# Kernel optimization log

Measured on AMD Instinct MI355X. Metric: run time of the kernel, lower is better.

The kernel has to match this reference:

```python
import jax, jax.numpy as jnp
import numpy as np

N, E = 50000, 800000
FN, FE, D, H = 64, 16, 128, 4


def setup_inputs() -> dict:
    key = jax.random.key(0)
    ks = jax.random.split(key, 16)
    inp = {
        "nodes": jax.random.normal(ks[0], (N, FN), jnp.float32),
        "edges": jax.random.normal(ks[1], (E, FE), jnp.float32),
        "senders": jax.random.randint(ks[2], (E,), 0, N, jnp.int32),
        "receivers": jax.random.randint(ks[3], (E,), 0, N, jnp.int32),
        "avg_multi_head": 0,
        # params (orthogonal init approximated by scaled normal; math identical)
        "W_node": jax.random.normal(ks[4], (FN, D), jnp.float32) / np.sqrt(FN),
        "b_node": jnp.zeros((D,), jnp.float32),
        "W_edge": jax.random.normal(ks[5], (FE, D), jnp.float32) / np.sqrt(FE),
        "b_edge": jnp.zeros((D,), jnp.float32),
        "Wk_s": jax.random.normal(ks[6], (H, D, D), jnp.float32) / np.sqrt(D),
        "bk_s": jnp.zeros((H, D), jnp.float32),
        "Wk_r": jax.random.normal(ks[7], (H, D, D), jnp.float32) / np.sqrt(D),
        "bk_r": jnp.zeros((H, D), jnp.float32),
        "W_out": jax.random.normal(ks[8], (H * D, D), jnp.float32) / np.sqrt(H * D),
        "b_out": jnp.zeros((D,), jnp.float32),
    }
    return inp


def _segment_softmax(logits, seg_ids, num_segments):
    seg_max = jax.ops.segment_max(logits, seg_ids, num_segments=num_segments)
    seg_max = jnp.where(jnp.isfinite(seg_max), seg_max, 0.0)  # empty segments
    e = jnp.exp(logits - seg_max[seg_ids])
    seg_sum = jax.ops.segment_sum(e, seg_ids, num_segments=num_segments)
    return e / seg_sum[seg_ids]


def reference(nodes, edges, senders, receivers, avg_multi_head,
              W_node, b_node, W_edge, b_edge, Wk_s, bk_s, Wk_r, bk_r,
              W_out, b_out):
    n_node = nodes.shape[0]
    x = nodes @ W_node + b_node            # [N, D] projected nodes
    ef = edges @ W_edge + b_edge           # [E, D] projected edge features
    sa = x[senders]                        # [E, D] sent attributes
    ra = x[receivers]                      # [E, D] received attributes
    scale = 1.0 / jnp.sqrt(jnp.asarray(D, x.dtype))
    heads = []
    for h in range(H):  # small fixed head count, structurally distinct params
        k_s = sa @ Wk_s[h] + bk_s[h]                 # [E, D]
        k_r = ra @ Wk_r[h] + bk_r[h] + ef            # [E, D]
        logits = jnp.sum(k_s * k_r, axis=1) * scale  # [E]
        w = _segment_softmax(logits, receivers, n_node)
        msg = w[:, None] * (sa + ef)                 # [E, D]
        heads.append(jax.ops.segment_sum(msg, receivers, num_segments=n_node))
    if avg_multi_head:
        agg = jnp.mean(jnp.stack(heads), axis=0)
    else:
        agg = jnp.concatenate(heads, axis=1) @ W_out + b_out
    return jax.nn.relu(x + agg)            # new node features [N, D]
```

## Files before the change

### kernel.cpp

```cpp
#include <hip/hip_runtime.h>

typedef unsigned short u16;
typedef unsigned int u32;
typedef short bh8 __attribute__((ext_vector_type(8)));
typedef float f4 __attribute__((ext_vector_type(4)));
typedef float pf2 __attribute__((ext_vector_type(2)));

__device__ __forceinline__ float bf2f(u16 h) { return __uint_as_float(((u32)h) << 16); }
__device__ __forceinline__ float bflo(u32 u) { return __uint_as_float(u << 16); }
__device__ __forceinline__ float bfhi(u32 u) { return __uint_as_float(u & 0xffff0000u); }
__device__ __forceinline__ u16 f2bf(float f) {
    u32 x = __float_as_uint(f);
    return (u16)((x + 0x7fffu + ((x >> 16) & 1u)) >> 16);
}
__device__ __forceinline__ pf2 pkfma(pf2 a, pf2 b, pf2 c) {
    pf2 d;
    asm("v_pk_fma_f32 %0, %1, %2, %3" : "=v"(d) : "v"(a), "v"(b), "v"(c));
    return d;
}
__device__ __forceinline__ pf2 u2f2(u32 u) {
    pf2 r;
    r.x = bflo(u);
    r.y = bfhi(u);
    return r;
}
__device__ __forceinline__ float dpp_red16(float x) {
    int y;
    y = __builtin_amdgcn_update_dpp(0, __float_as_int(x), 0xB1, 0xF, 0xF, true);
    x += __int_as_float(y);
    y = __builtin_amdgcn_update_dpp(0, __float_as_int(x), 0x4E, 0xF, 0xF, true);
    x += __int_as_float(y);
    y = __builtin_amdgcn_update_dpp(0, __float_as_int(x), 0x141, 0xF, 0xF, true);
    x += __int_as_float(y);
    y = __builtin_amdgcn_update_dpp(0, __float_as_int(x), 0x140, 0xF, 0xF, true);
    x += __int_as_float(y);
    return x;
}

#define KSCL 0.12751744336457488f

__global__ void k0a_kernel(const float* __restrict__ Wn, const float* __restrict__ Wks,
                           const float* __restrict__ Wkr, float* __restrict__ A,
                           float* __restrict__ B) {
    int idx = blockIdx.x * 256 + threadIdx.x;
    if (idx >= 65536) return;
    int which = idx >> 15;
    int rem = idx & 32767;
    int h = rem >> 13;
    int r = rem & 8191;
    int a = r >> 7, dp = r & 127;
    const float* W = which ? Wks : Wkr;
    float acc = 0.f;
    for (int d = 0; d < 128; ++d)
        acc += Wn[a * 128 + d] * W[(h * 128 + d) * 128 + dp];
    (which ? B : A)[(h * 64 + a) * 128 + dp] = acc;
}

__global__ void k0a2_kernel(const float* __restrict__ bn, const float* __restrict__ Wks,
                            const float* __restrict__ Wkr, const float* __restrict__ bks,
                            const float* __restrict__ bkr, float* __restrict__ ybs,
                            float* __restrict__ ybr) {
    int idx = blockIdx.x * 256 + threadIdx.x;
    if (idx >= 1024) return;
    int which = idx >> 9;
    int rem = idx & 511;
    int h = rem >> 7, dp = rem & 127;
    const float* W = which ? Wks : Wkr;
    const float* b = which ? bks : bkr;
    float acc = b[h * 128 + dp];
    for (int d = 0; d < 128; ++d) acc += bn[d] * W[(h * 128 + d) * 128 + dp];
    (which ? ybs : ybr)[h * 128 + dp] = acc;
}

__global__ void k0b_kernel(const float* __restrict__ Wn, const float* __restrict__ bn,
                           const float* __restrict__ A, const float* __restrict__ B,
                           const float* __restrict__ ybr, const float* __restrict__ ybs,
                           const float* __restrict__ Wks, const float* __restrict__ Wedge,
                           const float* __restrict__ bks, const float* __restrict__ bedge,
                           float* __restrict__ Wfold, float* __restrict__ biasrow) {
    int idx = blockIdx.x * 256 + threadIdx.x;
    if (idx >= 65 * 708) return;
    int a = idx / 708, c = idx % 708;
    float val;
    if (c < 128) {
        val = (a < 64) ? Wn[a * 128 + c] : bn[c];
    } else if (c < 640) {
        int h = (c - 128) >> 7, i = (c - 128) & 127;
        const float* rv = (a < 64) ? &A[(h * 64 + a) * 128] : &ybr[h * 128];
        float s = 0.f;
        for (int d = 0; d < 128; ++d) s += rv[d] * Wks[(h * 128 + i) * 128 + d];
        val = s;
    } else if (c < 704) {
        int k = (c - 640) >> 2, h = (c - 640) & 3;
        const float* rv = (a < 64) ? &B[(h * 64 + a) * 128] : &ybs[h * 128];
        float s = 0.f;
        for (int d = 0; d < 128; ++d) s += rv[d] * Wedge[k * 128 + d];
        val = s;
    } else {
        int h = c - 704;
        const float* rv = (a < 64) ? &B[(h * 64 + a) * 128] : &ybs[h * 128];
        float s = 0.f;
        for (int d = 0; d < 128; ++d) s += rv[d] * bedge[d];
        val = s;
    }
    if (a < 64) Wfold[(size_t)a * 708 + c] = val;
    else biasrow[c] = val;
}

__global__ void wconv_kernel(const float* __restrict__ Wfold, const float* __restrict__ Wout,
                             u16* __restrict__ WfT, u16* __restrict__ WoT) {
    int i = blockIdx.x * 256 + threadIdx.x;
    if (i < 768 * 64) {
        int c = i >> 6, k = i & 63;
        WfT[i] = f2bf(c < 708 ? Wfold[(size_t)k * 708 + c] : 0.f);
    }
    int j = i - 768 * 64;
    if (j >= 0 && j < 128 * 512) {
        int c = j >> 9, k = j & 511;
        WoT[j] = f2bf(Wout[(size_t)k * 128 + c]);
    }
}

__global__ __launch_bounds__(256) void g1_kernel(const float* __restrict__ nodes,
                                                 const u16* __restrict__ WfT,
                                                 const float* __restrict__ biasrow,
                                                 u16* __restrict__ Xc, u16* __restrict__ V,
                                                 u16* __restrict__ U, float* __restrict__ E0,
                                                 int N) {
    __shared__ u16 Asm[64][72];
    __shared__ u16 Bsm[128][72];
    int t = threadIdx.x;
    int r0 = blockIdx.x * 64, c0 = blockIdx.y * 128;
    {
        int row = t >> 2, cb = (t & 3) * 16;
        int r = r0 + row;
        u16 pk[16];
        if (r < N) {
            const float* src = &nodes[(size_t)r * 64 + cb];
#pragma unroll
            for (int q = 0; q < 16; ++q) pk[q] = f2bf(src[q]);
        } else {
#pragma unroll
            for (int q = 0; q < 16; ++q) pk[q] = 0;
        }
        *(uint4*)&Asm[row][cb] = *(const uint4*)&pk[0];
        *(uint4*)&Asm[row][cb + 8] = *(const uint4*)&pk[8];
    }
    {
        int col = t >> 1, ks = (t & 1) * 32;
        const u16* src = &WfT[(size_t)(c0 + col) * 64 + ks];
        uint4 v0 = *(const uint4*)src;
        uint4 v1 = *(const uint4*)(src + 8);
        uint4 v2 = *(const uint4*)(src + 16);
        uint4 v3 = *(const uint4*)(src + 24);
        *(uint4*)&Bsm[col][ks] = v0;
        *(uint4*)&Bsm[col][ks + 8] = v1;
        *(uint4*)&Bsm[col][ks + 16] = v2;
        *(uint4*)&Bsm[col][ks + 24] = v3;
    }
    __syncthreads();
    int lane = t & 63, wave = t >> 6;
    int wm = wave >> 1, wn = wave & 1;
    int lr = lane & 15, lk = lane >> 4;
    f4 acc[2][4] = {};
#pragma unroll
    for (int kk = 0; kk < 2; ++kk) {
        bh8 a[2], b[4];
#pragma unroll
        for (int am = 0; am < 2; ++am)
            a[am] = *(const bh8*)&Asm[wm * 32 + am * 16 + lr][kk * 32 + lk * 8];
#pragma unroll
        for (int bn = 0; bn < 4; ++bn)
            b[bn] = *(const bh8*)&Bsm[wn * 64 + bn * 16 + lr][kk * 32 + lk * 8];
#pragma unroll
        for (int am = 0; am < 2; ++am)
#pragma unroll
            for (int bn = 0; bn < 4; ++bn)
                acc[am][bn] = __builtin_amdgcn_mfma_f32_16x16x32_bf16(a[am], b[bn], acc[am][bn], 0, 0, 0);
    }
#pragma unroll
    for (int am = 0; am < 2; ++am)
#pragma unroll
        for (int bn = 0; bn < 4; ++bn) {
            int c = c0 + wn * 64 + bn * 16 + lr;
            if (c < 708) {
                float brow = biasrow[c];
#pragma unroll
                for (int q = 0; q < 4; ++q) {
                    int r = r0 + wm * 32 + am * 16 + lk * 4 + q;
                    if (r < N) {
                        float val = acc[am][bn][q] + brow;
                        if (c < 128) Xc[(size_t)r * 128 + c] = f2bf(val);
                        else if (c < 640) V[(size_t)r * 512 + (c - 128)] = f2bf(val * KSCL);
                        else if (c < 704) U[(size_t)r * 64 + (c - 640)] = f2bf(val * KSCL);
                        else E0[(size_t)r * 4 + (c - 704)] = exp2f(val * KSCL);
                    }
                }
            }
        }
}

__global__ void hist_kernel(const int* __restrict__ recv, int* __restrict__ deg, int E) {
    int e = blockIdx.x * 256 + threadIdx.x;
    if (e < E) atomicAdd(&deg[recv[e]], 1);
}

__global__ __launch_bounds__(1024) void scan1_kernel(const int* __restrict__ deg,
                                                     int* __restrict__ pre,
                                                     int* __restrict__ bsum, int N) {
    __shared__ int sm[1024];
    int b = blockIdx.x, t = threadIdx.x;
    int i = b * 1024 + t;
    int v = (i < N) ? deg[i] : 0;
    sm[t] = v;
    __syncthreads();
    for (int off = 1; off < 1024; off <<= 1) {
        int u = (t >= off) ? sm[t - off] : 0;
        __syncthreads();
        sm[t] += u;
        __syncthreads();
    }
    if (i < N) pre[i] = sm[t] - v;
    if (t == 1023) bsum[b] = sm[1023];
}

__global__ void scan2_kernel(int* __restrict__ bsum, int* __restrict__ boff, int nb) {
    int t = threadIdx.x;
    int own = (t < nb) ? bsum[t] : 0;
    int v = own;
#pragma unroll
    for (int off = 1; off < 64; off <<= 1) {
        int u = __shfl_up(v, off);
        if (t >= off) v += u;
    }
    if (t < nb) boff[t] = v - own;
    if (t == 63) boff[64] = v;
}

__global__ void scan3_kernel(const int* __restrict__ pre, const int* __restrict__ boff,
                             int* __restrict__ row_start, int* __restrict__ cursor, int N) {
    int i = blockIdx.x * 1024 + threadIdx.x;
    if (i < N) {
        int rsv = pre[i] + boff[i >> 10];
        row_start[i] = rsv;
        cursor[i] = rsv;
    }
    if (i == N) row_start[N] = boff[64];
}

__global__ void scatter_kernel(const int* __restrict__ recv, const int* __restrict__ senders,
                               int* __restrict__ cursor, int2* __restrict__ esp, int E) {
    int e = blockIdx.x * 256 + threadIdx.x;
    if (e < E) {
        int s = senders[e];
        int p = atomicAdd(&cursor[recv[e]], 1);
        esp[p] = make_int2(e, s);
    }
}

__global__ __launch_bounds__(256, 3) void en_kernel(const int* __restrict__ row_start,
                                                    const int2* __restrict__ esp,
                                                    const float* __restrict__ edges,
                                                    const u16* __restrict__ Xc,
                                                    const u16* __restrict__ V,
                                                    const u16* __restrict__ Uu,
                                                    const float* __restrict__ E0,
                                                    const float* __restrict__ W_edge,
                                                    const float* __restrict__ b_edge,
                                                    u16* __restrict__ agg, int N) {
    __shared__ float Wl[2048];
    int t = threadIdx.x;
    for (int i = t; i < 2048; i += 256) {
        int k = i >> 7, ch = i & 127;
        int pos = (k << 7) | ((((ch >> 1) & 3) << 5) | (((ch >> 3) & 15) << 1) | (ch & 1));
        Wl[pos] = W_edge[i];
    }
    __syncthreads();
    int lane = t & 63, wid = t >> 6;
    int g = lane >> 4, k16 = lane & 15;
    int nw = blockIdx.x * 4 + wid;
    int NW = gridDim.x * 4;

#define IDX8(ea, sa, eb, sb, s_)                                            \
    {                                                                       \
        int ev = 0, sv = 0;                                                 \
        if (lane < 8) {                                                     \
            int jj = (s_)*8 + lane;                                         \
            if (jj >= deg) jj = deg - 1;                                    \
            int2 pv = esp[rs + jj];                                         \
            ev = pv.x; sv = pv.y;                                           \
        }                                                                   \
        ea = __shfl(ev, g); sa = __shfl(sv, g);                             \
        eb = __shfl(ev, 4 + g); sb = __shfl(sv, 4 + g);                     \
    }

#define LOADP(Xq, Uq, Eq, Zq, eI, sI)                                       \
    {                                                                       \
        Xq = *(const uint4*)(Xc + (size_t)(sI)*128 + 8 * k16);              \
        Uq = *(const uint2*)(Uu + (size_t)(sI)*64 + k16 * 4);               \
        Eq = edges[(size_t)(eI)*16 + k16];                                  \
        Zq = *(const float4*)(E0 + (size_t)(sI)*4);                         \
    }

#define COMP(Xq, Uq, Eq, Zq, act)                                           \
    {                                                                       \
        pf2 X0 = u2f2(Xq.x), X1 = u2f2(Xq.y), X2 = u2f2(Xq.z), X3 = u2f2(Xq.w); \
        float uh[4] = {bflo(Uq.x), bfhi(Uq.x), bflo(Uq.y), bfhi(Uq.y)};     \
        float e0a[4] = {Zq.x, Zq.y, Zq.z, Zq.w};                            \
        _Pragma("unroll") for (int h = 0; h < 4; ++h) {                     \
            pf2 p2 = {Eq * uh[h], 0.f};                                     \
            p2 = pkfma(X0, vr[h][0], p2); p2 = pkfma(X1, vr[h][1], p2);     \
            p2 = pkfma(X2, vr[h][2], p2); p2 = pkfma(X3, vr[h][3], p2);     \
            float p = dpp_red16(p2.x + p2.y);                               \
            float wh = (act) ? e0a[h] * exp2f(p) : 0.f;                     \
            Ss[h] += wh; aE[h] = fmaf(wh, Eq, aE[h]);                       \
            pf2 w2 = {wh, wh};                                              \
            aX[h][0] = pkfma(w2, X0, aX[h][0]);                             \
            aX[h][1] = pkfma(w2, X1, aX[h][1]);                             \
            aX[h][2] = pkfma(w2, X2, aX[h][2]);                             \
            aX[h][3] = pkfma(w2, X3, aX[h][3]);                             \
        }                                                                   \
    }

    for (int n = nw; n < N; n += NW) {
        int rs = row_start[n];
        int deg = row_start[n + 1] - rs;
        const u16* Vr = V + (size_t)n * 512;
        pf2 vr[4][4];
#pragma unroll
        for (int h = 0; h < 4; ++h) {
            uint4 v = *(const uint4*)(Vr + h * 128 + 8 * k16);
            vr[h][0] = u2f2(v.x); vr[h][1] = u2f2(v.y);
            vr[h][2] = u2f2(v.z); vr[h][3] = u2f2(v.w);
        }
        pf2 aX[4][4] = {};
        float Ss[4] = {0.f, 0.f, 0.f, 0.f};
        float aE[4] = {0.f, 0.f, 0.f, 0.f};

        if (deg > 0) {
            int nst = (deg + 7) >> 3;
            int eA0, sA0, eA1, sA1, eB0, sB0, eB1, sB1;
            IDX8(eA0, sA0, eA1, sA1, 0);
            uint4 xP0, xP1; uint2 uP0, uP1; float eP0, eP1; float4 zP0, zP1;
            LOADP(xP0, uP0, eP0, zP0, eA0, sA0);
            LOADP(xP1, uP1, eP1, zP1, eA1, sA1);
            if (nst > 1) {
                IDX8(eB0, sB0, eB1, sB1, 1);
            } else {
                eB0 = eA0; sB0 = sA0; eB1 = eA1; sB1 = sA1;
            }
            for (int s = 0; s < nst; ++s) {
                uint4 xc0 = xP0, xc1 = xP1;
                uint2 uc0 = uP0, uc1 = uP1;
                float ec0 = eP0, ec1 = eP1;
                float4 zc0 = zP0, zc1 = zP1;
                int base = s * 8;
                if (s + 1 < nst) {
                    LOADP(xP0, uP0, eP0, zP0, eB0, sB0);
                    LOADP(xP1, uP1, eP1, zP1, eB1, sB1);
                    if (s + 2 < nst) IDX8(eB0, sB0, eB1, sB1, s + 2);
                }
                COMP(xc0, uc0, ec0, zc0, base + g < deg);
                COMP(xc1, uc1, ec1, zc1, base + 4 + g < deg);
            }
        }
#pragma unroll
        for (int h = 0; h < 4; ++h) {
#pragma unroll
            for (int i = 0; i < 4; ++i) {
                pf2 v = aX[h][i];
                v.x += __shfl_xor(v.x, 16); v.y += __shfl_xor(v.y, 16);
                v.x += __shfl_xor(v.x, 32); v.y += __shfl_xor(v.y, 32);
                aX[h][i] = v;
            }
            Ss[h] += __shfl_xor(Ss[h], 16); Ss[h] += __shfl_xor(Ss[h], 32);
            aE[h] += __shfl_xor(aE[h], 16); aE[h] += __shfl_xor(aE[h], 32);
        }
        pf2 axg[4];
#pragma unroll
        for (int i = 0; i < 4; ++i)
            axg[i] = g == 0 ? aX[0][i] : g == 1 ? aX[1][i] : g == 2 ? aX[2][i] : aX[3][i];
        float aEg = g == 0 ? aE[0] : g == 1 ? aE[1] : g == 2 ? aE[2] : aE[3];
        float Sg = g == 0 ? Ss[0] : g == 1 ? Ss[1] : g == 2 ? Ss[2] : Ss[3];
        const pf2* Wp = (const pf2*)Wl;
#pragma unroll
        for (int kk = 0; kk < 16; ++kk) {
            float a = __shfl(aEg, (g << 4) | kk);
            pf2 a2 = {a, a};
            int base = (kk << 6) + k16;
            axg[0] = pkfma(a2, Wp[base], axg[0]);
            axg[1] = pkfma(a2, Wp[base + 16], axg[1]);
            axg[2] = pkfma(a2, Wp[base + 32], axg[2]);
            axg[3] = pkfma(a2, Wp[base + 48], axg[3]);
        }
        {
            float inv = (deg > 0 && Sg > 0.f) ? 1.f / Sg : 0.f;
            float bes = (deg > 0) ? 1.f : 0.f;
            const float* br = &b_edge[8 * k16];
            u32 o0 = (u32)f2bf(axg[0].x * inv + bes * br[0]) |
                     ((u32)f2bf(axg[0].y * inv + bes * br[1]) << 16);
            u32 o1 = (u32)f2bf(axg[1].x * inv + bes * br[2]) |
                     ((u32)f2bf(axg[1].y * inv + bes * br[3]) << 16);
            u32 o2 = (u32)f2bf(axg[2].x * inv + bes * br[4]) |
                     ((u32)f2bf(axg[2].y * inv + bes * br[5]) << 16);
            u32 o3 = (u32)f2bf(axg[3].x * inv + bes * br[6]) |
                     ((u32)f2bf(axg[3].y * inv + bes * br[7]) << 16);
            uint4 st = {o0, o1, o2, o3};
            *(uint4*)(agg + (size_t)n * 512 + g * 128 + 8 * k16) = st;
        }
    }
#undef IDX8
#undef LOADP
#undef COMP
}

__global__ __launch_bounds__(256) void g3_kernel(const u16* __restrict__ Xc,
                                                 const u16* __restrict__ agg,
                                                 const u16* __restrict__ WoT,
                                                 const float* __restrict__ bout,
                                                 const int* __restrict__ avgflag,
                                                 float* __restrict__ out, int N) {
    int t = threadIdx.x;
    int r0 = blockIdx.x * 64;
    if (*avgflag) {
        for (int i = t; i < 64 * 128; i += 256) {
            int n = r0 + (i >> 7), j = i & 127;
            if (n < N) {
                float s = 0.f;
#pragma unroll
                for (int h = 0; h < 4; ++h) s += bf2f(agg[(size_t)n * 512 + h * 128 + j]);
                float v = bf2f(Xc[(size_t)n * 128 + j]) + 0.25f * s;
                out[(size_t)n * 128 + j] = v > 0.f ? v : 0.f;
            }
        }
        return;
    }
    __shared__ u16 Asm[64][72];
    __shared__ u16 Bsm[128][72];
    int lane = t & 63, wave = t >> 6;
    int wm = wave >> 1, wn = wave & 1;
    int lr = lane & 15, lk = lane >> 4;
    f4 acc[2][4] = {};
    for (int kb = 0; kb < 8; ++kb) {
        if (kb) __syncthreads();
        {
            int row = t >> 2, ks = (t & 3) * 16;
            int r = r0 + row;
            uint4 v0 = {0, 0, 0, 0}, v1 = {0, 0, 0, 0};
            if (r < N) {
                const u16* src = &agg[(size_t)r * 512 + kb * 64 + ks];
                v0 = *(const uint4*)src;
                v1 = *(const uint4*)(src + 8);
            }
            *(uint4*)&Asm[row][ks] = v0;
            *(uint4*)&Asm[row][ks + 8] = v1;
        }
        {
            int col = t >> 1, ks = (t & 1) * 32;
            const u16* src = &WoT[(size_t)col * 512 + kb * 64 + ks];
            uint4 v0 = *(const uint4*)src;
            uint4 v1 = *(const uint4*)(src + 8);
            uint4 v2 = *(const uint4*)(src + 16);
            uint4 v3 = *(const uint4*)(src + 24);
            *(uint4*)&Bsm[col][ks] = v0;
            *(uint4*)&Bsm[col][ks + 8] = v1;
            *(uint4*)&Bsm[col][ks + 16] = v2;
            *(uint4*)&Bsm[col][ks + 24] = v3;
        }
        __syncthreads();
#pragma unroll
        for (int kk = 0; kk < 2; ++kk) {
            bh8 a[2], b[4];
#pragma unroll
            for (int am = 0; am < 2; ++am)
                a[am] = *(const bh8*)&Asm[wm * 32 + am * 16 + lr][kk * 32 + lk * 8];
#pragma unroll
            for (int bn = 0; bn < 4; ++bn)
                b[bn] = *(const bh8*)&Bsm[wn * 64 + bn * 16 + lr][kk * 32 + lk * 8];
#pragma unroll
            for (int am = 0; am < 2; ++am)
#pragma unroll
                for (int bn = 0; bn < 4; ++bn)
                    acc[am][bn] = __builtin_amdgcn_mfma_f32_16x16x32_bf16(a[am], b[bn], acc[am][bn], 0, 0, 0);
        }
    }
#pragma unroll
    for (int am = 0; am < 2; ++am)
#pragma unroll
        for (int bn = 0; bn < 4; ++bn) {
            int c = wn * 64 + bn * 16 + lr;
            float bc = bout[c];
#pragma unroll
            for (int q = 0; q < 4; ++q) {
                int r = r0 + wm * 32 + am * 16 + lk * 4 + q;
                if (r < N) {
                    float v = acc[am][bn][q] + bc + bf2f(Xc[(size_t)r * 128 + c]);
                    out[(size_t)r * 128 + c] = v > 0.f ? v : 0.f;
                }
            }
        }
}

extern "C" void kernel_launch(void* const* d_in, const int* in_sizes, int n_in, void* d_out,
                              int out_size, void* d_ws, size_t ws_size, hipStream_t stream) {
    const float* nodes = (const float*)d_in[0];
    const float* edges = (const float*)d_in[1];
    const int* senders = (const int*)d_in[2];
    const int* receivers = (const int*)d_in[3];
    const int* avgflag = (const int*)d_in[4];
    const float* W_node = (const float*)d_in[5];
    const float* b_node = (const float*)d_in[6];
    const float* W_edge = (const float*)d_in[7];
    const float* b_edge = (const float*)d_in[8];
    const float* Wk_s = (const float*)d_in[9];
    const float* bk_s = (const float*)d_in[10];
    const float* Wk_r = (const float*)d_in[11];
    const float* bk_r = (const float*)d_in[12];
    const float* W_out = (const float*)d_in[13];
    const float* b_out = (const float*)d_in[14];
    int N = in_sizes[0] / 64;
    int E = in_sizes[2];
    float* outp = (float*)d_out;

    char* base = (char*)d_ws;
    size_t off = 0;
    auto alloc = [&](size_t nbytes) -> char* {
        char* p = base + off;
        off = (off + nbytes + 255) & ~(size_t)255;
        return p;
    };
    u16* Xc = (u16*)alloc((size_t)N * 128 * 2);
    u16* V = (u16*)alloc((size_t)N * 512 * 2);
    u16* U = (u16*)alloc((size_t)N * 64 * 2);
    float* E0 = (float*)alloc((size_t)N * 4 * 4);
    u16* agg = (u16*)alloc((size_t)N * 512 * 2);
    int* deg = (int*)alloc((size_t)N * 4);
    int* row_start = (int*)alloc((size_t)(N + 1) * 4);
    int* cursor = (int*)alloc((size_t)N * 4);
    int2* esp = (int2*)alloc((size_t)E * 8);
    int* pre = (int*)alloc((size_t)N * 4);
    int* bsum = (int*)alloc((size_t)128 * 4);
    int* boff = (int*)alloc((size_t)128 * 4);
    float* A = (float*)alloc((size_t)4 * 64 * 128 * 4);
    float* B = (float*)alloc((size_t)4 * 64 * 128 * 4);
    float* ybr = (float*)alloc((size_t)4 * 128 * 4);
    float* ybs = (float*)alloc((size_t)4 * 128 * 4);
    float* Wfold = (float*)alloc((size_t)64 * 708 * 4);
    float* biasrow = (float*)alloc((size_t)712 * 4);
    u16* WfT = (u16*)alloc((size_t)768 * 64 * 2);
    u16* WoT = (u16*)alloc((size_t)128 * 512 * 2);

    int nb = (N + 1023) >> 10;

    hipMemsetAsync(deg, 0, (size_t)N * 4, stream);
    k0a_kernel<<<256, 256, 0, stream>>>(W_node, Wk_s, Wk_r, A, B);
    k0a2_kernel<<<4, 256, 0, stream>>>(b_node, Wk_s, Wk_r, bk_s, bk_r, ybs, ybr);
    k0b_kernel<<<(65 * 708 + 255) / 256, 256, 0, stream>>>(W_node, b_node, A, B, ybr, ybs,
                                                           Wk_s, W_edge, bk_s, b_edge, Wfold,
                                                           biasrow);
    wconv_kernel<<<(768 * 64 + 128 * 512 + 255) / 256, 256, 0, stream>>>(Wfold, W_out, WfT, WoT);
    dim3 g1grid((N + 63) / 64, 6);
    g1_kernel<<<g1grid, 256, 0, stream>>>(nodes, WfT, biasrow, Xc, V, U, E0, N);
    hist_kernel<<<(E + 255) / 256, 256, 0, stream>>>(receivers, deg, E);
    scan1_kernel<<<nb, 1024, 0, stream>>>(deg, pre, bsum, N);
    scan2_kernel<<<1, 64, 0, stream>>>(bsum, boff, nb);
    scan3_kernel<<<(N + 1024) / 1024, 1024, 0, stream>>>(pre, boff, row_start, cursor, N);
    scatter_kernel<<<(E + 255) / 256, 256, 0, stream>>>(receivers, senders, cursor, esp, E);
    en_kernel<<<4096, 256, 0, stream>>>(row_start, esp, edges, Xc, V, U, E0, W_edge,
                                        b_edge, agg, N);
    g3_kernel<<<(N + 63) / 64, 256, 0, stream>>>(Xc, agg, WoT, b_out, avgflag, outp, N);
}
```

Baseline: 331.0 us.

## Prefetch next node's row bounds, V rows and first edges across node iterations

```diff
diff --git a/kernel.cpp b/kernel.cpp
--- a/kernel.cpp
+++ b/kernel.cpp
@@ -258,7 +258,7 @@
     }
 }
 
-__global__ __launch_bounds__(256, 3) void en_kernel(const int* __restrict__ row_start,
+__global__ __launch_bounds__(256, 4) void en_kernel(const int* __restrict__ row_start,
                                                     const int2* __restrict__ esp,
                                                     const float* __restrict__ edges,
                                                     const u16* __restrict__ Xc,
@@ -280,19 +280,6 @@
     int g = lane >> 4, k16 = lane & 15;
     int nw = blockIdx.x * 4 + wid;
     int NW = gridDim.x * 4;
-
-#define IDX8(ea, sa, eb, sb, s_)                                            \
-    {                                                                       \
-        int ev = 0, sv = 0;                                                 \
-        if (lane < 8) {                                                     \
-            int jj = (s_)*8 + lane;                                         \
-            if (jj >= deg) jj = deg - 1;                                    \
-            int2 pv = esp[rs + jj];                                         \
-            ev = pv.x; sv = pv.y;                                           \
-        }                                                                   \
-        ea = __shfl(ev, g); sa = __shfl(sv, g);                             \
-        eb = __shfl(ev, 4 + g); sb = __shfl(sv, 4 + g);                     \
-    }
 
 #define LOADP(Xq, Uq, Eq, Zq, eI, sI)                                       \
     {                                                                       \
@@ -322,16 +309,61 @@
         }                                                                   \
     }
 
-    for (int n = nw; n < N; n += NW) {
-        int rs = row_start[n];
-        int deg = row_start[n + 1] - rs;
+    int n = nw;
+    if (n >= N) return;
+    int rs = row_start[n], re = row_start[n + 1];
+    uint4 vn0, vn1, vn2, vn3;
+    {
         const u16* Vr = V + (size_t)n * 512;
+        vn0 = *(const uint4*)(Vr + 0 * 128 + 8 * k16);
+        vn1 = *(const uint4*)(Vr + 1 * 128 + 8 * k16);
+        vn2 = *(const uint4*)(Vr + 2 * 128 + 8 * k16);
+        vn3 = *(const uint4*)(Vr + 3 * 128 + 8 * k16);
+    }
+    int eB0, sB0, eB1, sB1;
+    uint4 xP0, xP1;
+    uint2 uP0, uP1;
+    float eP0, eP1;
+    float4 zP0, zP1;
+    {
+        int deg = re - rs;
+        int2 pvA = {0, 0}, pvB = {0, 0};
+        if (lane < 8 && deg > 0) {
+            int jj = lane;
+            if (jj >= deg) jj = deg - 1;
+            pvA = esp[rs + jj];
+            int jj2 = 8 + lane;
+            if (jj2 >= deg) jj2 = deg - 1;
+            pvB = esp[rs + jj2];
+        }
+        int eA0 = __shfl(pvA.x, g), sA0 = __shfl(pvA.y, g);
+        int eA1 = __shfl(pvA.x, 4 + g), sA1 = __shfl(pvA.y, 4 + g);
+        eB0 = __shfl(pvB.x, g); sB0 = __shfl(pvB.y, g);
+        eB1 = __shfl(pvB.x, 4 + g); sB1 = __shfl(pvB.y, 4 + g);
+        LOADP(xP0, uP0, eP0, zP0, eA0, sA0);
+        LOADP(xP1, uP1, eP1, zP1, eA1, sA1);
+    }
+
+    while (true) {
+        int deg = re - rs;
+        int n2 = n + NW;
+        bool more = (n2 < N);
+        int rs2 = 0, re2 = 0;
+        if (more) {
+            rs2 = row_start[n2];
+            re2 = row_start[n2 + 1];
+        }
         pf2 vr[4][4];
-#pragma unroll
-        for (int h = 0; h < 4; ++h) {
-            uint4 v = *(const uint4*)(Vr + h * 128 + 8 * k16);
-            vr[h][0] = u2f2(v.x); vr[h][1] = u2f2(v.y);
-            vr[h][2] = u2f2(v.z); vr[h][3] = u2f2(v.w);
+        vr[0][0] = u2f2(vn0.x); vr[0][1] = u2f2(vn0.y); vr[0][2] = u2f2(vn0.z); vr[0][3] = u2f2(vn0.w);
+        vr[1][0] = u2f2(vn1.x); vr[1][1] = u2f2(vn1.y); vr[1][2] = u2f2(vn1.z); vr[1][3] = u2f2(vn1.w);
+        vr[2][0] = u2f2(vn2.x); vr[2][1] = u2f2(vn2.y); vr[2][2] = u2f2(vn2.z); vr[2][3] = u2f2(vn2.w);
+        vr[3][0] = u2f2(vn3.x); vr[3][1] = u2f2(vn3.y); vr[3][2] = u2f2(vn3.z); vr[3][3] = u2f2(vn3.w);
+        {
+            const u16* Vr = V + (size_t)(more ? n2 : n) * 512;
+            vn0 = *(const uint4*)(Vr + 0 * 128 + 8 * k16);
+            vn1 = *(const uint4*)(Vr + 1 * 128 + 8 * k16);
+            vn2 = *(const uint4*)(Vr + 2 * 128 + 8 * k16);
+            vn3 = *(const uint4*)(Vr + 3 * 128 + 8 * k16);
         }
         pf2 aX[4][4] = {};
         float Ss[4] = {0.f, 0.f, 0.f, 0.f};
@@ -339,16 +371,6 @@
 
         if (deg > 0) {
             int nst = (deg + 7) >> 3;
-            int eA0, sA0, eA1, sA1, eB0, sB0, eB1, sB1;
-            IDX8(eA0, sA0, eA1, sA1, 0);
-            uint4 xP0, xP1; uint2 uP0, uP1; float eP0, eP1; float4 zP0, zP1;
-            LOADP(xP0, uP0, eP0, zP0, eA0, sA0);
-            LOADP(xP1, uP1, eP1, zP1, eA1, sA1);
-            if (nst > 1) {
-                IDX8(eB0, sB0, eB1, sB1, 1);
-            } else {
-                eB0 = eA0; sB0 = sA0; eB1 = eA1; sB1 = sA1;
-            }
             for (int s = 0; s < nst; ++s) {
                 uint4 xc0 = xP0, xc1 = xP1;
                 uint2 uc0 = uP0, uc1 = uP1;
@@ -358,10 +380,31 @@
                 if (s + 1 < nst) {
                     LOADP(xP0, uP0, eP0, zP0, eB0, sB0);
                     LOADP(xP1, uP1, eP1, zP1, eB1, sB1);
-                    if (s + 2 < nst) IDX8(eB0, sB0, eB1, sB1, s + 2);
+                    if (s + 2 < nst) {
+                        int2 pv = {0, 0};
+                        if (lane < 8) {
+                            int jj = (s + 2) * 8 + lane;
+                            if (jj >= deg) jj = deg - 1;
+                            pv = esp[rs + jj];
+                        }
+                        eB0 = __shfl(pv.x, g); sB0 = __shfl(pv.y, g);
+                        eB1 = __shfl(pv.x, 4 + g); sB1 = __shfl(pv.y, 4 + g);
+                    }
                 }
                 COMP(xc0, uc0, ec0, zc0, base + g < deg);
                 COMP(xc1, uc1, ec1, zc1, base + 4 + g < deg);
+            }
+        }
+        int2 pvA = {0, 0}, pvB = {0, 0};
+        if (more) {
+            int deg2 = re2 - rs2;
+            if (lane < 8 && deg2 > 0) {
+                int jj = lane;
+                if (jj >= deg2) jj = deg2 - 1;
+                pvA = esp[rs2 + jj];
+                int jj2 = 8 + lane;
+                if (jj2 >= deg2) jj2 = deg2 - 1;
+                pvB = esp[rs2 + jj2];
             }
         }
 #pragma unroll
@@ -408,8 +451,17 @@
             uint4 st = {o0, o1, o2, o3};
             *(uint4*)(agg + (size_t)n * 512 + g * 128 + 8 * k16) = st;
         }
-    }
-#undef IDX8
+        if (!more) break;
+        {
+            int eA0 = __shfl(pvA.x, g), sA0 = __shfl(pvA.y, g);
+            int eA1 = __shfl(pvA.x, 4 + g), sA1 = __shfl(pvA.y, 4 + g);
+            eB0 = __shfl(pvB.x, g); sB0 = __shfl(pvB.y, g);
+            eB1 = __shfl(pvB.x, 4 + g); sB1 = __shfl(pvB.y, 4 + g);
+            LOADP(xP0, uP0, eP0, zP0, eA0, sA0);
+            LOADP(xP1, uP1, eP1, zP1, eA1, sA1);
+        }
+        n = n2; rs = rs2; re = re2;
+    }
 #undef LOADP
 #undef COMP
 }
```

Result: slower. 522.7 us (+57.9%).
